# Performance work log

Measured on AMD Instinct MI355X. Metric: run time of the kernel, lower is better.

Reference implementation:

```python
import jax, jax.numpy as jnp
import numpy as np

B, S, DIM = 2, 2048, 2048
NH, NKV = 16, 16
HD = 128            # constructor head_dim (full per-head dim, = 2 * self.head_dim)
HHD = HD // 2       # self.head_dim = per-stream dim = 64
ROPE_THETA = 10000.0
LAMBDA_INIT = 0.8 - 0.6 * float(np.exp(-0.3 * 0))  # block_id = 0 -> 0.2
EPS = 1e-5


def make_freq_cis(seq_len, dim, theta):
    # rotation matrices, shape (seq, dim//2, 2, 2): [[cos, -sin], [sin, cos]]
    inv = 1.0 / (theta ** (np.arange(0, dim, 2, dtype=np.float32) / dim))
    ang = np.arange(seq_len, dtype=np.float32)[:, None] * inv[None, :]
    cos, sin = np.cos(ang), np.sin(ang)
    fc = np.stack([np.stack([cos, -sin], -1), np.stack([sin, cos], -1)], -2)
    return jnp.asarray(fc, dtype=jnp.float32)


def setup_inputs() -> dict:
    key = jax.random.key(0)
    ks = jax.random.split(key, 9)
    std = DIM ** -0.5
    return {
        "x": jax.random.normal(ks[0], (B, S, DIM), jnp.float32),
        "freq_cis": make_freq_cis(S, HD, ROPE_THETA),
        "wq": jax.random.normal(ks[1], (NH * HD, DIM), jnp.float32) * std,
        "wk": jax.random.normal(ks[2], (NKV * HD, DIM), jnp.float32) * std,
        "wv": jax.random.normal(ks[3], (NKV * HD, DIM), jnp.float32) * std,
        "wo": jax.random.normal(ks[4], (DIM, NH * HD), jnp.float32) * std,
        "lambda_q1": jax.random.normal(ks[5], (HHD,), jnp.float32) * 0.1,
        "lambda_k1": jax.random.normal(ks[6], (HHD,), jnp.float32) * 0.1,
        "lambda_q2": jax.random.normal(ks[7], (HHD,), jnp.float32) * 0.1,
        "lambda_k2": jax.random.normal(ks[8], (HHD,), jnp.float32) * 0.1,
        "subln_w": jnp.ones((HD,), jnp.float32),
    }


def _rope(t, fc):
    # t: (b, s, h, d); fc: (s, d//2, 2, 2). Pairs (even, odd) rotated by 2x2 matrix.
    b, s, h, d = t.shape
    t2 = t.reshape(b, s, h, d // 2, 1, 2)
    out = (t2 * fc[None, :, None]).sum(-1)  # (b, s, h, d//2, 2)
    return out.reshape(b, s, h, d)


def _causal_attn(q, k, v):
    # q, k: (b, s, h, HHD); v: (b, s, h, HD). Flash-attn default scale = 1/sqrt(q head dim).
    scale = 1.0 / jnp.sqrt(jnp.asarray(q.shape[-1], q.dtype))
    scores = jnp.einsum('bqhd,bkhd->bhqk', q, k) * scale
    s = q.shape[1]
    causal = jnp.tril(jnp.ones((s, s), bool))
    scores = jnp.where(causal, scores, jnp.finfo(scores.dtype).min)
    p = jax.nn.softmax(scores, axis=-1)
    return jnp.einsum('bhqk,bkhd->bqhd', p, v)  # (b, s, h, HD)


def reference(x, freq_cis, wq, wk, wv, wo, lambda_q1, lambda_k1, lambda_q2, lambda_k2, subln_w):
    b, s, _ = x.shape
    xq = (x @ wq.T).reshape(b, s, NH, HD)
    xk = (x @ wk.T).reshape(b, s, NKV, HD)
    xv = (x @ wv.T).reshape(b, s, NKV, HD)
    xq = _rope(xq, freq_cis)
    xk = _rope(xk, freq_cis)
    if NKV != NH:  # GQA: repeat kv heads group-wise
        rep = NH // NKV
        xk = jnp.repeat(xk, rep, axis=2)
        xv = jnp.repeat(xv, rep, axis=2)
    # split each head into two differential streams of size HHD
    xq = xq.reshape(b, s, NH, 2, HHD)
    xk = xk.reshape(b, s, NH, 2, HHD)
    attn1 = _causal_attn(xq[:, :, :, 0], xk[:, :, :, 0], xv)
    attn2 = _causal_attn(xq[:, :, :, 1], xk[:, :, :, 1], xv)
    lam1 = jnp.exp(jnp.sum(lambda_q1 * lambda_k1))
    lam2 = jnp.exp(jnp.sum(lambda_q2 * lambda_k2))
    lam_full = lam1 - lam2 + LAMBDA_INIT
    attn = attn1 - lam_full * attn2              # (b, s, h, HD)
    attn = jnp.transpose(attn, (0, 2, 1, 3))     # faithful to torch .transpose(1, 2)
    ms = jnp.mean(jnp.square(attn), axis=-1, keepdims=True)
    attn = attn * jax.lax.rsqrt(ms + EPS) * subln_w  # RMSNorm(2*HHD)
    attn = attn * (1.0 - LAMBDA_INIT)
    # faithful to original: reshape (b, h, s, HD) row-major into (b, s, h*HD)
    attn = attn.reshape(b, s, NH * HD)
    return attn @ wo.T
```

## Files before the change

### kernel.cpp

```cpp
#include <hip/hip_runtime.h>

typedef unsigned short u16;
typedef unsigned int   u32;
typedef __attribute__((ext_vector_type(8))) short s16x8;
typedef __attribute__((ext_vector_type(4))) float f32x4;

constexpr int Bc = 2, Sc = 2048, DIMc = 2048, NHc = 16, HDc = 128, Tc = Bc * Sc;
constexpr float LAMBDA_INIT_C = 0.2f;

__device__ __forceinline__ u16 f2bf(float f) {
  union { float f; u32 u; } v; v.f = f;
  u32 r = v.u + 0x7fffu + ((v.u >> 16) & 1u);
  return (u16)(r >> 16);
}
__device__ __forceinline__ float bf2f(u16 b) {
  union { u32 u; float f; } v; v.u = ((u32)b) << 16;
  return v.f;
}
__device__ __forceinline__ f32x4 mfma16(s16x8 a, s16x8 b, f32x4 c) {
  return __builtin_amdgcn_mfma_f32_16x16x32_bf16(a, b, c, 0, 0, 0);
}

typedef const __attribute__((address_space(1))) u32 gq32;
typedef __attribute__((address_space(3))) u32 lq32;
__device__ __forceinline__ void cp16(const u16* g, u16* l) {
  __builtin_amdgcn_global_load_lds((gq32*)g, (lq32*)l, 16, 0, 0);
}

__global__ void cvt_all_kernel(const float* __restrict__ x,
                               const float* __restrict__ wq, const float* __restrict__ wk,
                               const float* __restrict__ wv, const float* __restrict__ wo,
                               u16* __restrict__ xb, u16* __restrict__ wb) {
  const int i = blockIdx.x * 256 + threadIdx.x;
  constexpr int NX = Tc * DIMc / 4;
  constexpr int PW = DIMc * DIMc / 4;
  float4 v; uint2* dst;
  if (i < NX) {
    v = ((const float4*)x)[i];
    dst = ((uint2*)xb) + i;
  } else {
    const int j = i - NX;
    const int which = j >> 20;
    const int jj = j & (PW - 1);
    const float* src = which == 0 ? wq : which == 1 ? wk : which == 2 ? wv : wo;
    v = ((const float4*)src)[jj];
    dst = ((uint2*)wb) + j;
  }
  union { u16 u[4]; uint2 p; } o;
  o.u[0] = f2bf(v.x); o.u[1] = f2bf(v.y); o.u[2] = f2bf(v.z); o.u[3] = f2bf(v.w);
  *dst = o.p;
}

__global__ __launch_bounds__(256) void gemm_qkv(const u16* __restrict__ A,
                                                const u16* __restrict__ Wq,
                                                const u16* __restrict__ Wk,
                                                const u16* __restrict__ Wv,
                                                u16* __restrict__ Oq,
                                                u16* __restrict__ Ok,
                                                u16* __restrict__ Ov) {
  constexpr int K = DIMc, N = DIMc;
  __shared__ u16 lA[128 * 32];
  __shared__ u16 lB[128 * 32];
  const int nglob = blockIdx.x * 128;
  const int which = nglob >> 11;
  const u16* Bw = which == 0 ? Wq : which == 1 ? Wk : Wv;
  u16*       Cb = which == 0 ? Oq : which == 1 ? Ok : Ov;
  const int nbase = nglob & (N - 1);
  const int mbase = blockIdx.y * 128;

  const int tid  = threadIdx.x;
  const int lane = tid & 63;
  const int w    = tid >> 6;
  const int wrow = (w >> 1) * 64;
  const int wcol = (w & 1) * 64;
  const int l15  = lane & 15;
  const int quad = lane >> 4;

  f32x4 acc[4][4];
#pragma unroll
  for (int i = 0; i < 4; i++)
#pragma unroll
    for (int j = 0; j < 4; j++) acc[i][j] = (f32x4){0.f, 0.f, 0.f, 0.f};

  const int srow = w * 32 + (lane >> 2);
  const int scol = (lane & 3) * 8;
  const u16* gA = A  + (size_t)(mbase + srow) * K + scol;
  const u16* gB = Bw + (size_t)(nbase + srow) * K + scol;
  u16* sA = lA + srow * 32 + scol;
  u16* sB = lB + srow * 32 + scol;

  for (int kb = 0; kb < K; kb += 32) {
    __syncthreads();
    cp16(gA + kb,                  sA);
    cp16(gA + kb + (size_t)16 * K, sA + 16 * 32);
    cp16(gB + kb,                  sB);
    cp16(gB + kb + (size_t)16 * K, sB + 16 * 32);
    __syncthreads();
    s16x8 af[4], bfr[4];
#pragma unroll
    for (int i = 0; i < 4; i++)
      af[i] = *(const s16x8*)(lA + (wrow + i * 16 + l15) * 32 + quad * 8);
#pragma unroll
    for (int j = 0; j < 4; j++)
      bfr[j] = *(const s16x8*)(lB + (wcol + j * 16 + l15) * 32 + quad * 8);
#pragma unroll
    for (int i = 0; i < 4; i++)
#pragma unroll
      for (int j = 0; j < 4; j++) acc[i][j] = mfma16(af[i], bfr[j], acc[i][j]);
  }

#pragma unroll
  for (int i = 0; i < 4; i++) {
    const int m0 = mbase + wrow + i * 16 + quad * 4;
#pragma unroll
    for (int j = 0; j < 4; j++) {
      const int n0 = nbase + wcol + j * 16 + l15;
#pragma unroll
      for (int r = 0; r < 4; r++) Cb[(size_t)(m0 + r) * N + n0] = f2bf(acc[i][j][r]);
    }
  }
}

__global__ __launch_bounds__(256) void gemm_bt(const u16* __restrict__ A,
                                               const u16* __restrict__ Bw,
                                               float* __restrict__ Cf,
                                               int M, int N, int K) {
  __shared__ u16 lA[128 * 32];
  __shared__ u16 lB[128 * 32];
  const int tid  = threadIdx.x;
  const int lane = tid & 63;
  const int w    = tid >> 6;
  const int mbase = blockIdx.y * 128;
  const int nbase = blockIdx.x * 128;
  const int wrow = (w >> 1) * 64;
  const int wcol = (w & 1) * 64;
  const int l15  = lane & 15;
  const int quad = lane >> 4;

  f32x4 acc[4][4];
#pragma unroll
  for (int i = 0; i < 4; i++)
#pragma unroll
    for (int j = 0; j < 4; j++) acc[i][j] = (f32x4){0.f, 0.f, 0.f, 0.f};

  const int srow = w * 32 + (lane >> 2);
  const int scol = (lane & 3) * 8;
  const u16* gA = A  + (size_t)(mbase + srow) * K + scol;
  const u16* gB = Bw + (size_t)(nbase + srow) * K + scol;
  u16* sA = lA + srow * 32 + scol;
  u16* sB = lB + srow * 32 + scol;

  for (int kb = 0; kb < K; kb += 32) {
    __syncthreads();
    cp16(gA + kb,                  sA);
    cp16(gA + kb + (size_t)16 * K, sA + 16 * 32);
    cp16(gB + kb,                  sB);
    cp16(gB + kb + (size_t)16 * K, sB + 16 * 32);
    __syncthreads();
    s16x8 af[4], bfr[4];
#pragma unroll
    for (int i = 0; i < 4; i++)
      af[i] = *(const s16x8*)(lA + (wrow + i * 16 + l15) * 32 + quad * 8);
#pragma unroll
    for (int j = 0; j < 4; j++)
      bfr[j] = *(const s16x8*)(lB + (wcol + j * 16 + l15) * 32 + quad * 8);
#pragma unroll
    for (int i = 0; i < 4; i++)
#pragma unroll
      for (int j = 0; j < 4; j++) acc[i][j] = mfma16(af[i], bfr[j], acc[i][j]);
  }

#pragma unroll
  for (int i = 0; i < 4; i++) {
    const int m0 = mbase + wrow + i * 16 + quad * 4;
#pragma unroll
    for (int j = 0; j < 4; j++) {
      const int n0 = nbase + wcol + j * 16 + l15;
#pragma unroll
      for (int r = 0; r < 4; r++) Cf[(size_t)(m0 + r) * N + n0] = acc[i][j][r];
    }
  }
}

__global__ void prep_kernel(const u16* __restrict__ qg, const u16* __restrict__ kg,
                            const u16* __restrict__ vg, const float* __restrict__ fc,
                            u16* __restrict__ qr, u16* __restrict__ kr,
                            u16* __restrict__ vt) {
  __shared__ u16 tile[32][33];
  const int bid = blockIdx.x;
  if (bid < 32768) {
    const bool isq = bid < 16384;
    const u16* xg = isq ? qg : kg;
    u16* outp = isq ? qr : kr;
    const float scale = isq ? 0.125f : 1.0f;
    const int idx = (bid & 16383) * 256 + threadIdx.x;
    const int p = idx & 63;
    const int hh = (idx >> 6) & 15;
    const int tt = idx >> 10;
    const int s = tt & (Sc - 1);
    const int bb = tt >> 11;
    const float c  = fc[(size_t)(s * 64 + p) * 4 + 0] * scale;
    const float sn = fc[(size_t)(s * 64 + p) * 4 + 2] * scale;
    const u32 xp = *(const u32*)(xg + (size_t)tt * DIMc + hh * HDc + p * 2);
    const float x0 = bf2f((u16)xp), x1 = bf2f((u16)(xp >> 16));
    const u16 y0 = f2bf(c * x0 - sn * x1);
    const u16 y1 = f2bf(sn * x0 + c * x1);
    *(u32*)(outp + ((size_t)(bb * NHc + hh) * Sc + s) * HDc + p * 2) =
        (u32)y0 | ((u32)y1 << 16);
  } else {
    const int vb = bid - 32768;
    const int bh = vb >> 8;
    const int bb = bh >> 4, hh = bh & 15;
    const int rem = vb & 255;
    const int s0 = (rem & 63) * 32, d0 = (rem >> 6) * 32;
    const int tx = threadIdx.x & 31, ty = threadIdx.x >> 5;
#pragma unroll
    for (int pp = 0; pp < 4; pp++) {
      const int s = s0 + ty + pp * 8;
      tile[ty + pp * 8][tx] = vg[(size_t)(bb * Sc + s) * DIMc + hh * HDc + d0 + tx];
    }
    __syncthreads();
#pragma unroll
    for (int pp = 0; pp < 4; pp++) {
      const int d = d0 + ty + pp * 8;
      vt[((size_t)bh * HDc + d) * Sc + s0 + tx] = tile[tx][ty + pp * 8];
    }
  }
}

__global__ __launch_bounds__(256, 2) void diff_attn_kernel(
    const u16* __restrict__ qr, const u16* __restrict__ kr, const u16* __restrict__ vt,
    const float* __restrict__ lq1, const float* __restrict__ lk1,
    const float* __restrict__ lq2, const float* __restrict__ lk2,
    const float* __restrict__ subw, u16* __restrict__ Y) {
  __shared__ u16 KB[2][8192];
  __shared__ u16 VB[2][8192];

  const int h = blockIdx.y, b = blockIdx.z, jb = blockIdx.x;
  const int bh = b * NHc + h;
  const int tid = threadIdx.x;
  const int w = tid >> 6, lane = tid & 63;
  const int l15 = lane & 15, quad = lane >> 4;

  const u16* krb = kr + (size_t)bh * Sc * HDc;
  const u16* vtb = vt + (size_t)bh * HDc * Sc;

  float lp1 = lq1[lane] * lk1[lane];
  float lp2 = lq2[lane] * lk2[lane];
#pragma unroll
  for (int m = 32; m; m >>= 1) { lp1 += __shfl_xor(lp1, m); lp2 += __shfl_xor(lp2, m); }
  const float lam = __expf(lp1) - __expf(lp2) + LAMBDA_INIT_C;

  float wsub[8];
#pragma unroll
  for (int dn = 0; dn < 8; dn++) wsub[dn] = subw[dn * 16 + l15];

  size_t offK[4], offV[4];
  int dstO[4];
#pragma unroll
  for (int oo = 0; oo < 4; oo++) {
    const int n = w * 256 + oo * 64 + lane;
    const int s = n & 31, dblk = (n >> 5) & 15, sub = n >> 9;
    const int mkey = (s & 3) + ((s >> 2) & 3) * 8 + ((s >> 4) << 2);
    offK[oo] = (size_t)(sub * 32 + mkey) * HDc + dblk * 8;
    offV[oo] = (size_t)(n & 127) * Sc + (sub * 32 + ((n >> 7) & 3) * 8);
    dstO[oo] = n * 8;
  }

  for (int ph = 0; ph < 2; ph++) {
    const int t = ph ? (31 - jb) : jb;
    const int rowbase = t * 64 + w * 16;
    const int nc = t + 1;

    const u16* qp = qr + ((size_t)bh * Sc + rowbase + l15) * HDc + quad * 8;
    s16x8 qa[2][2];
    qa[0][0] = *(const s16x8*)(qp);
    qa[0][1] = *(const s16x8*)(qp + 32);
    qa[1][0] = *(const s16x8*)(qp + 64);
    qa[1][1] = *(const s16x8*)(qp + 96);

    f32x4 o[2][8];
#pragma unroll
    for (int st = 0; st < 2; st++)
#pragma unroll
      for (int dn = 0; dn < 8; dn++) o[st][dn] = (f32x4){0.f, 0.f, 0.f, 0.f};
    float lpart[2] = { 0.f, 0.f };

    __syncthreads();
#pragma unroll
    for (int oo = 0; oo < 4; oo++) cp16(krb + offK[oo], KB[0] + dstO[oo]);
#pragma unroll
    for (int oo = 0; oo < 4; oo++) cp16(vtb + offV[oo], VB[0] + dstO[oo]);

    for (int c = 0; c < nc; c++) {
      __syncthreads();
      if (c + 1 < nc) {
        const int kb1 = (c + 1) * 64;
        u16* Kn = KB[(c + 1) & 1];
        u16* Vn = VB[(c + 1) & 1];
#pragma unroll
        for (int oo = 0; oo < 4; oo++) cp16(krb + (size_t)kb1 * HDc + offK[oo], Kn + dstO[oo]);
#pragma unroll
        for (int oo = 0; oo < 4; oo++) cp16(vtb + offV[oo] + kb1, Vn + dstO[oo]);
      }
      const u16* Kb = KB[c & 1];
      const u16* Vb = VB[c & 1];
      const int kb = c * 64;
      const bool diag = (c == nc - 1);

#pragma unroll
      for (int sub = 0; sub < 2; sub++) {
        if (diag && sub == 1 && w < 2) continue;

        f32x4 sc[2][2];
#pragma unroll
        for (int st = 0; st < 2; st++)
#pragma unroll
          for (int kt = 0; kt < 2; kt++) sc[st][kt] = (f32x4){0.f, 0.f, 0.f, 0.f};
#pragma unroll
        for (int st = 0; st < 2; st++)
#pragma unroll
          for (int kh = 0; kh < 2; kh++) {
            const int base = sub * 512 + (st * 8 + kh * 4 + quad) * 32;
#pragma unroll
            for (int kt = 0; kt < 2; kt++) {
              const s16x8 kf = *(const s16x8*)(Kb + (size_t)(base + kt * 16 + l15) * 8);
              sc[st][kt] = mfma16(kf, qa[st][kh], sc[st][kt]);
            }
          }

        s16x8 pa[2];
#pragma unroll
        for (int st = 0; st < 2; st++) {
          float p[8];
#pragma unroll
          for (int kt = 0; kt < 2; kt++)
#pragma unroll
            for (int r = 0; r < 4; r++) p[kt * 4 + r] = __expf(sc[st][kt][r]);
          if (diag) {
            const int qrow = rowbase + l15;
            const int kb0 = kb + sub * 32 + quad * 8;
#pragma unroll
            for (int j8 = 0; j8 < 8; j8++)
              if (kb0 + j8 > qrow) p[j8] = 0.f;
          }
          float sm = 0.f;
#pragma unroll
          for (int j8 = 0; j8 < 8; j8++) sm += p[j8];
          lpart[st] += sm;
          union { u16 us[8]; s16x8 vv; } pk;
#pragma unroll
          for (int j8 = 0; j8 < 8; j8++) pk.us[j8] = f2bf(p[j8]);
          pa[st] = pk.vv;
        }

#pragma unroll
        for (int dn = 0; dn < 8; dn++) {
          const s16x8 vf =
              *(const s16x8*)(Vb + (size_t)(sub * 512 + quad * 128 + dn * 16 + l15) * 8);
          o[0][dn] = mfma16(pa[0], vf, o[0][dn]);
          o[1][dn] = mfma16(pa[1], vf, o[1][dn]);
        }
      }
    }

    float lL0 = lpart[0], lL1 = lpart[1];
    lL0 += __shfl_xor(lL0, 16); lL0 += __shfl_xor(lL0, 32);
    lL1 += __shfl_xor(lL1, 16); lL1 += __shfl_xor(lL1, 32);
    const float inv1 = 1.f / lL0;
    const float inv2 = lam / lL1;
    float i1C[4], i2C[4];
#pragma unroll
    for (int r = 0; r < 4; r++) {
      i1C[r] = __shfl(inv1, quad * 4 + r, 16);
      i2C[r] = __shfl(inv2, quad * 4 + r, 16);
    }
    float yv[8][4], ss[4] = { 0.f, 0.f, 0.f, 0.f };
#pragma unroll
    for (int dn = 0; dn < 8; dn++)
#pragma unroll
      for (int r = 0; r < 4; r++) {
        const float y = o[0][dn][r] * i1C[r] - o[1][dn][r] * i2C[r];
        yv[dn][r] = y;
        ss[r] += y * y;
      }
#pragma unroll
    for (int r = 0; r < 4; r++) {
#pragma unroll
      for (int mm = 1; mm < 16; mm <<= 1) ss[r] += __shfl_xor(ss[r], mm);
    }
    float scl[4];
#pragma unroll
    for (int r = 0; r < 4; r++) scl[r] = rsqrtf(ss[r] * (1.f / 128.f) + 1e-5f) * 0.8f;

    u16* yrow = Y + ((size_t)(b * Sc + h * 128 + t * 4 + w)) * 2048;
#pragma unroll
    for (int dn = 0; dn < 8; dn++)
#pragma unroll
      for (int r = 0; r < 4; r++)
        yrow[(quad * 4 + r) * 128 + dn * 16 + l15] = f2bf(yv[dn][r] * scl[r] * wsub[dn]);
  }
}

extern "C" void kernel_launch(void* const* d_in, const int* in_sizes, int n_in,
                              void* d_out, int out_size, void* d_ws, size_t ws_size,
                              hipStream_t stream) {
  const float* x    = (const float*)d_in[0];
  const float* fc   = (const float*)d_in[1];
  const float* wq   = (const float*)d_in[2];
  const float* wk   = (const float*)d_in[3];
  const float* wv   = (const float*)d_in[4];
  const float* wo   = (const float*)d_in[5];
  const float* lq1  = (const float*)d_in[6];
  const float* lk1  = (const float*)d_in[7];
  const float* lq2  = (const float*)d_in[8];
  const float* lk2  = (const float*)d_in[9];
  const float* subw = (const float*)d_in[10];
  float* out = (float*)d_out;

  char* ws = (char*)d_ws;
  constexpr size_t SZ_X  = (size_t)Tc * DIMc * 2;
  constexpr size_t SZ_W  = (size_t)DIMc * DIMc * 2;
  constexpr size_t SZ_T  = (size_t)Tc * DIMc * 2;
  u16* xb  = (u16*)(ws);
  u16* wqb = (u16*)(ws + SZ_X);
  u16* wkb = (u16*)(ws + SZ_X + SZ_W);
  u16* wvb = (u16*)(ws + SZ_X + 2 * SZ_W);
  u16* wob = (u16*)(ws + SZ_X + 3 * SZ_W);
  u16* qg  = (u16*)(ws + SZ_X + 4 * SZ_W);
  u16* kg  = (u16*)(ws + SZ_X + 4 * SZ_W + SZ_T);
  u16* vg  = (u16*)(ws + SZ_X + 4 * SZ_W + 2 * SZ_T);
  u16* qr  = (u16*)(ws + SZ_X + 4 * SZ_W + 3 * SZ_T);
  u16* kr  = (u16*)(ws + SZ_X + 4 * SZ_W + 4 * SZ_T);
  u16* vt  = (u16*)(ws + SZ_X + 4 * SZ_W + 5 * SZ_T);
  u16* Y   = (u16*)(ws + SZ_X + 4 * SZ_W + 6 * SZ_T);

  cvt_all_kernel<<<(Tc * DIMc / 4 + 4 * DIMc * DIMc / 4) / 256, 256, 0, stream>>>(
      x, wq, wk, wv, wo, xb, wqb);

  gemm_qkv<<<dim3(48, Tc / 128), 256, 0, stream>>>(xb, wqb, wkb, wvb, qg, kg, vg);

  prep_kernel<<<16384 + 16384 + 8192, 256, 0, stream>>>(qg, kg, vg, fc, qr, kr, vt);

  diff_attn_kernel<<<dim3(16, NHc, Bc), 256, 0, stream>>>(
      qr, kr, vt, lq1, lk1, lq2, lk2, subw, Y);

  gemm_bt<<<dim3(DIMc / 128, Tc / 128), 256, 0, stream>>>(Y, wob, out, Tc, DIMc, DIMc);
}
```

Baseline: 437.9 us.

## Fuse RoPE, Q scaling and V transpose into QKV GEMM epilogue

Removes the separate prep kernel by applying RoPE (with a lane shuffle to fetch the rotation partner) and the query scale directly on the GEMM accumulators. V is written transposed straight from the accumulators. This avoids writing and re-reading three T×DIM bf16 intermediates and one kernel launch. In exchange the epilogue does scattered fc loads and writes that are less coalesced, with 2-byte stores for Q/K and 8-byte stores along the sequence dimension for V.

```diff
diff --git a/kernel.cpp b/kernel.cpp
--- a/kernel.cpp
+++ b/kernel.cpp
@@ -55,16 +55,16 @@
                                                 const u16* __restrict__ Wq,
                                                 const u16* __restrict__ Wk,
                                                 const u16* __restrict__ Wv,
-                                                u16* __restrict__ Oq,
-                                                u16* __restrict__ Ok,
-                                                u16* __restrict__ Ov) {
+                                                const float* __restrict__ fc,
+                                                u16* __restrict__ qr,
+                                                u16* __restrict__ kr,
+                                                u16* __restrict__ vt) {
   constexpr int K = DIMc, N = DIMc;
   __shared__ u16 lA[128 * 32];
   __shared__ u16 lB[128 * 32];
   const int nglob = blockIdx.x * 128;
   const int which = nglob >> 11;
   const u16* Bw = which == 0 ? Wq : which == 1 ? Wk : Wv;
-  u16*       Cb = which == 0 ? Oq : which == 1 ? Ok : Ov;
   const int nbase = nglob & (N - 1);
   const int mbase = blockIdx.y * 128;
 
@@ -109,14 +109,44 @@
       for (int j = 0; j < 4; j++) acc[i][j] = mfma16(af[i], bfr[j], acc[i][j]);
   }
 
-#pragma unroll
-  for (int i = 0; i < 4; i++) {
-    const int m0 = mbase + wrow + i * 16 + quad * 4;
-#pragma unroll
-    for (int j = 0; j < 4; j++) {
-      const int n0 = nbase + wcol + j * 16 + l15;
-#pragma unroll
-      for (int r = 0; r < 4; r++) Cb[(size_t)(m0 + r) * N + n0] = f2bf(acc[i][j][r]);
+  const int hh = nbase >> 7;
+  const int bb = mbase >> 11;
+  const size_t bhOff = (size_t)(bb * NHc + hh);
+
+  if (which < 2) {
+    u16* outp = which == 0 ? qr : kr;
+    const float scale = which == 0 ? 0.125f : 1.0f;
+#pragma unroll
+    for (int i = 0; i < 4; i++) {
+      const int m0 = mbase + wrow + i * 16 + quad * 4;
+#pragma unroll
+      for (int j = 0; j < 4; j++) {
+        const int d = wcol + j * 16 + l15;
+        const int p = d >> 1;
+        const float sign = (d & 1) ? 1.f : -1.f;
+#pragma unroll
+        for (int r = 0; r < 4; r++) {
+          const int s = (m0 + r) & (Sc - 1);
+          const float4 f4 = *(const float4*)(fc + (size_t)(s * 64 + p) * 4);
+          const float c = f4.x * scale, sn = f4.z * scale;
+          const float xv = acc[i][j][r];
+          const float prt = __shfl_xor(xv, 1);
+          outp[(bhOff * Sc + s) * HDc + d] = f2bf(c * xv + sign * sn * prt);
+        }
+      }
+    }
+  } else {
+#pragma unroll
+    for (int i = 0; i < 4; i++) {
+      const int s0 = (mbase + wrow + i * 16 + quad * 4) & (Sc - 1);
+#pragma unroll
+      for (int j = 0; j < 4; j++) {
+        const int d = wcol + j * 16 + l15;
+        union { u16 u[4]; uint2 pck; } o4;
+#pragma unroll
+        for (int r = 0; r < 4; r++) o4.u[r] = f2bf(acc[i][j][r]);
+        *(uint2*)(vt + (bhOff * HDc + d) * Sc + s0) = o4.pck;
+      }
     }
   }
 }
@@ -182,52 +212,6 @@
   }
 }
 
-__global__ void prep_kernel(const u16* __restrict__ qg, const u16* __restrict__ kg,
-                            const u16* __restrict__ vg, const float* __restrict__ fc,
-                            u16* __restrict__ qr, u16* __restrict__ kr,
-                            u16* __restrict__ vt) {
-  __shared__ u16 tile[32][33];
-  const int bid = blockIdx.x;
-  if (bid < 32768) {
-    const bool isq = bid < 16384;
-    const u16* xg = isq ? qg : kg;
-    u16* outp = isq ? qr : kr;
-    const float scale = isq ? 0.125f : 1.0f;
-    const int idx = (bid & 16383) * 256 + threadIdx.x;
-    const int p = idx & 63;
-    const int hh = (idx >> 6) & 15;
-    const int tt = idx >> 10;
-    const int s = tt & (Sc - 1);
-    const int bb = tt >> 11;
-    const float c  = fc[(size_t)(s * 64 + p) * 4 + 0] * scale;
-    const float sn = fc[(size_t)(s * 64 + p) * 4 + 2] * scale;
-    const u32 xp = *(const u32*)(xg + (size_t)tt * DIMc + hh * HDc + p * 2);
-    const float x0 = bf2f((u16)xp), x1 = bf2f((u16)(xp >> 16));
-    const u16 y0 = f2bf(c * x0 - sn * x1);
-    const u16 y1 = f2bf(sn * x0 + c * x1);
-    *(u32*)(outp + ((size_t)(bb * NHc + hh) * Sc + s) * HDc + p * 2) =
-        (u32)y0 | ((u32)y1 << 16);
-  } else {
-    const int vb = bid - 32768;
-    const int bh = vb >> 8;
-    const int bb = bh >> 4, hh = bh & 15;
-    const int rem = vb & 255;
-    const int s0 = (rem & 63) * 32, d0 = (rem >> 6) * 32;
-    const int tx = threadIdx.x & 31, ty = threadIdx.x >> 5;
-#pragma unroll
-    for (int pp = 0; pp < 4; pp++) {
-      const int s = s0 + ty + pp * 8;
-      tile[ty + pp * 8][tx] = vg[(size_t)(bb * Sc + s) * DIMc + hh * HDc + d0 + tx];
-    }
-    __syncthreads();
-#pragma unroll
-    for (int pp = 0; pp < 4; pp++) {
-      const int d = d0 + ty + pp * 8;
-      vt[((size_t)bh * HDc + d) * Sc + s0 + tx] = tile[tx][ty + pp * 8];
-    }
-  }
-}
-
 __global__ __launch_bounds__(256, 2) void diff_attn_kernel(
     const u16* __restrict__ qr, const u16* __restrict__ kr, const u16* __restrict__ vt,
     const float* __restrict__ lq1, const float* __restrict__ lk1,
@@ -427,20 +411,15 @@
   u16* wkb = (u16*)(ws + SZ_X + SZ_W);
   u16* wvb = (u16*)(ws + SZ_X + 2 * SZ_W);
   u16* wob = (u16*)(ws + SZ_X + 3 * SZ_W);
-  u16* qg  = (u16*)(ws + SZ_X + 4 * SZ_W);
-  u16* kg  = (u16*)(ws + SZ_X + 4 * SZ_W + SZ_T);
-  u16* vg  = (u16*)(ws + SZ_X + 4 * SZ_W + 2 * SZ_T);
-  u16* qr  = (u16*)(ws + SZ_X + 4 * SZ_W + 3 * SZ_T);
-  u16* kr  = (u16*)(ws + SZ_X + 4 * SZ_W + 4 * SZ_T);
-  u16* vt  = (u16*)(ws + SZ_X + 4 * SZ_W + 5 * SZ_T);
-  u16* Y   = (u16*)(ws + SZ_X + 4 * SZ_W + 6 * SZ_T);
+  u16* qr  = (u16*)(ws + SZ_X + 4 * SZ_W);
+  u16* kr  = (u16*)(ws + SZ_X + 4 * SZ_W + SZ_T);
+  u16* vt  = (u16*)(ws + SZ_X + 4 * SZ_W + 2 * SZ_T);
+  u16* Y   = (u16*)(ws + SZ_X + 4 * SZ_W + 3 * SZ_T);
 
   cvt_all_kernel<<<(Tc * DIMc / 4 + 4 * DIMc * DIMc / 4) / 256, 256, 0, stream>>>(
       x, wq, wk, wv, wo, xb, wqb);
 
-  gemm_qkv<<<dim3(48, Tc / 128), 256, 0, stream>>>(xb, wqb, wkb, wvb, qg, kg, vg);
-
-  prep_kernel<<<16384 + 16384 + 8192, 256, 0, stream>>>(qg, kg, vg, fc, qr, kr, vt);
+  gemm_qkv<<<dim3(48, Tc / 128), 256, 0, stream>>>(xb, wqb, wkb, wvb, fc, qr, kr, vt);
 
   diff_attn_kernel<<<dim3(16, NHc, Bc), 256, 0, stream>>>(
       qr, kr, vt, lq1, lk1, lq2, lk2, subw, Y);
```

After: 443.6 us. No clear change (+1.3%).
